# Kernel tuning notes

Measured on AMD Instinct MI355X. Metric: run time of the kernel, lower is better.

The kernel has to match this reference:

```python
import jax, jax.numpy as jnp
import numpy as np

N = 50000          # nodes
E = 400000         # edges
MUL = 32           # multiplicity per irrep
NUM_NEIGHBORS = 8.0
INV_SQRT3 = 1.0 / np.sqrt(3.0)  # w3j(1,1,0) coefficient


def setup_inputs() -> dict:
    key = jax.random.key(0)
    ks = jax.random.split(key, 20)
    inp = {
        # node_input: 32x0e (dim 32) + 32x1o (dim 96) = 128
        "node_input": jax.random.normal(ks[0], (N, 4 * MUL), jnp.float32),
        "node_attr": jnp.ones((N, 1), jnp.float32),           # 1x0e trivial attr
        "edge_src": jax.random.randint(ks[1], (E,), 0, N, jnp.int32),
        "edge_dst": jax.random.randint(ks[2], (E,), 0, N, jnp.int32),
        "edge_attr": jax.random.normal(ks[3], (E, 4), jnp.float32),   # 1x0e + 1x1o
        "edge_scalars": jax.random.normal(ks[4], (E, 16), jnp.float32),
        # FullyConnectedTensorProduct weights (uvw, node_attr has mul 1)
        "w_sc0": jax.random.normal(ks[5], (MUL, MUL), jnp.float32),
        "w_sc1": jax.random.normal(ks[6], (MUL, MUL), jnp.float32),
        "w_lin1_0": jax.random.normal(ks[7], (MUL, MUL), jnp.float32),
        "w_lin1_1": jax.random.normal(ks[8], (MUL, MUL), jnp.float32),
        # radial FC net -> per-edge TP weights (numel = 4*MUL = 128)
        "fc_w1": jax.random.normal(ks[9], (16, 64), jnp.float32),
        "fc_w2": jax.random.normal(ks[10], (64, 4 * MUL), jnp.float32),
        # lin2: irreps_mid (64x0e+64x1o) x attr -> output
        "w_lin2_0": jax.random.normal(ks[11], (2 * MUL, MUL), jnp.float32),
        "w_lin2_1": jax.random.normal(ks[12], (2 * MUL, MUL), jnp.float32),
        # alpha: irreps_mid x attr -> 0e (zero-init in original; small randn for a nontrivial test)
        "w_alpha": 0.1 * jax.random.normal(ks[13], (2 * MUL, 1), jnp.float32),
        # sc_edges: irreps_mid x edge_attr -> edge_attr
        "w_se0a": jax.random.normal(ks[14], (2 * MUL,), jnp.float32),  # mid0e x ea0e -> 0e
        "w_se0b": jax.random.normal(ks[15], (2 * MUL,), jnp.float32),  # mid1o x ea1o -> 0e
        "w_se1a": jax.random.normal(ks[16], (2 * MUL,), jnp.float32),  # mid0e x ea1o -> 1o
        "w_se1b": jax.random.normal(ks[17], (2 * MUL,), jnp.float32),  # mid1o x ea0e -> 1o
    }
    return inp


def reference(node_input, node_attr, edge_src, edge_dst, edge_attr, edge_scalars,
              w_sc0, w_sc1, w_lin1_0, w_lin1_1, fc_w1, fc_w2,
              w_lin2_0, w_lin2_1, w_alpha, w_se0a, w_se0b, w_se1a, w_se1b):
    inv_nn = 1.0 / jnp.sqrt(jnp.asarray(NUM_NEIGHBORS, node_input.dtype))
    n = node_input.shape[0]
    x0 = node_input[:, :MUL]                       # (N, 32)   32x0e
    x1 = node_input[:, MUL:].reshape(n, MUL, 3)    # (N, 32, 3) 32x1o
    a = node_attr                                  # (N, 1)
    s_in = 1.0 / np.sqrt(MUL)                      # FCTP fan-in normalization

    # self-connection: FCTP(input, attr) -> output
    sc0 = (x0 @ w_sc0) * a * s_in
    sc1 = jnp.einsum('num,uw->nwm', x1, w_sc1) * a[:, :, None] * s_in
    node_self = jnp.concatenate([sc0, sc1.reshape(n, 3 * MUL)], axis=1)  # (N, 128)

    # lin1: FCTP(input, attr) -> input irreps
    f0 = (x0 @ w_lin1_0) * a * s_in
    f1 = jnp.einsum('num,uw->nwm', x1, w_lin1_1) * a[:, :, None] * s_in

    # gather source node features per edge
    g0 = f0[edge_src]                              # (E, 32)
    g1 = f1[edge_src]                              # (E, 32, 3)
    ea0 = edge_attr[:, :1]                         # (E, 1)   1x0e
    ea1 = edge_attr[:, 1:]                         # (E, 3)   1x1o

    # radial net -> per-edge TP weights (FullyConnectedNet with sin activation)
    h = jnp.sin(edge_scalars @ fc_w1 * (1.0 / np.sqrt(16.0)))
    w = h @ fc_w2 * (1.0 / np.sqrt(64.0))          # (E, 128)
    wA, wB, wC, wD = jnp.split(w, 4, axis=1)       # each (E, 32)

    # uvu tensor product, 4 instructions
    mA = wA * g0 * ea0                                           # 0e x 0e -> 0e
    mD = wD * jnp.einsum('eum,em->eu', g1, ea1) * INV_SQRT3      # 1o x 1o -> 0e
    mB = (wB * g0)[:, :, None] * ea1[:, None, :]                 # 0e x 1o -> 1o
    mC = (wC[:, :, None] * g1) * ea0[:, :, None]                 # 1o x 0e -> 1o
    mid0 = jnp.concatenate([mA, mD], axis=1)       # (E, 64)  64x0e
    mid1 = jnp.concatenate([mB, mC], axis=1)       # (E, 64, 3) 64x1o

    # scatter-add to destination nodes
    n0 = jax.ops.segment_sum(mid0, edge_dst, num_segments=n) * inv_nn
    n1 = jax.ops.segment_sum(mid1, edge_dst, num_segments=n) * inv_nn

    s_mid = 1.0 / np.sqrt(2 * MUL)
    out0 = (n0 @ w_lin2_0) * a * s_mid
    out1 = jnp.einsum('num,uw->nwm', n1, w_lin2_1) * a[:, :, None] * s_mid
    node_conv = jnp.concatenate([out0, out1.reshape(n, 3 * MUL)], axis=1)

    # alpha gate (sc.output_mask is all ones here, so alpha = 1 - 1 + alpha*1)
    alpha = (n0 @ w_alpha) * a * s_mid             # (N, 1)
    node_conv_out = node_self + alpha * node_conv  # (N, 128)

    # sc_edges: FCTP(mid, edge_attr) -> edge_attr irreps; fan-in = 128 per output
    s_se = 1.0 / np.sqrt(4 * MUL)
    se0 = ((mid0 @ w_se0a) * ea0[:, 0]
           + jnp.einsum('eum,em,u->e', mid1, ea1, w_se0b) * INV_SQRT3) * s_se
    se1 = ((mid0 @ w_se1a)[:, None] * ea1
           + jnp.einsum('eum,u->em', mid1, w_se1b) * ea0) * s_se
    edge_conv_out = edge_attr + jnp.concatenate([se0[:, None], se1], axis=1) * inv_nn

    return node_conv_out, edge_conv_out
```

## Files before the change

kernel.cpp:

```cpp
#include <hip/hip_runtime.h>
#include <math.h>

#define N_NODES 50000
#define E_EDGES 400000

typedef _Float16 f16x2 __attribute__((ext_vector_type(2)));
typedef _Float16 f16x4 __attribute__((ext_vector_type(4)));
typedef _Float16 f16x8 __attribute__((ext_vector_type(8)));

static constexpr float S_IN      = 0.17677669529663687f;
static constexpr float S_MID     = 0.125f;
static constexpr float S_SE      = 0.08838834764831843f;
static constexpr float INV_NN    = 0.35355339059327373f;
static constexpr float INV_SQRT3 = 0.5773502691896258f;
static constexpr float FC1_S     = 0.25f;
static constexpr float FC2_S     = 0.125f;

__device__ inline float dot2(f16x2 a, f16x2 b, float c) {
#if __has_builtin(__builtin_amdgcn_fdot2)
    return __builtin_amdgcn_fdot2(a, b, c, false);
#else
    return c + (float)a[0] * (float)b[0] + (float)a[1] * (float)b[1];
#endif
}

__device__ inline float wave_reduce_dpp(float v) {
    int x;
    x = __builtin_amdgcn_update_dpp(0, __float_as_int(v), 0x111, 0xf, 0xf, true); v += __int_as_float(x);
    x = __builtin_amdgcn_update_dpp(0, __float_as_int(v), 0x112, 0xf, 0xf, true); v += __int_as_float(x);
    x = __builtin_amdgcn_update_dpp(0, __float_as_int(v), 0x114, 0xf, 0xf, true); v += __int_as_float(x);
    x = __builtin_amdgcn_update_dpp(0, __float_as_int(v), 0x118, 0xf, 0xf, true); v += __int_as_float(x);
    x = __builtin_amdgcn_update_dpp(0, __float_as_int(v), 0x142, 0xa, 0xf, true); v += __int_as_float(x);
    x = __builtin_amdgcn_update_dpp(0, __float_as_int(v), 0x143, 0xc, 0xf, true); v += __int_as_float(x);
    return __int_as_float(__builtin_amdgcn_readlane(__float_as_int(v), 63));
}

__global__ __launch_bounds__(256) void node_pre_kernel(
    const float* __restrict__ node_input, const float* __restrict__ node_attr,
    const float* __restrict__ w_sc0, const float* __restrict__ w_sc1,
    const float* __restrict__ w_lin1_0, const float* __restrict__ w_lin1_1,
    float* __restrict__ out_self, float* __restrict__ ws_f)
{
    const int n0 = blockIdx.x * 8;
    const int t  = threadIdx.x;
    __shared__ __align__(16) float sx[8 * 128];
    __shared__ float sa[8];
    ((float4*)sx)[t] = ((const float4*)(node_input + (size_t)n0 * 128))[t];
    if (t < 8) sa[t] = node_attr[n0 + t];
    __syncthreads();

    const int half = t >> 7;
    const int idx  = t & 127;
    float wcol[32];
    int m = 0;
    if (idx < 32) {
        const float* __restrict__ W = half ? w_lin1_0 : w_sc0;
        #pragma unroll
        for (int u = 0; u < 32; ++u) wcol[u] = W[u * 32 + idx];
    } else {
        const float* __restrict__ W = half ? w_lin1_1 : w_sc1;
        const int j = idx - 32;
        const int w = j / 3; m = j % 3;
        #pragma unroll
        for (int u = 0; u < 32; ++u) wcol[u] = W[u * 32 + w];
    }
    float* __restrict__ dstp = half ? ws_f : out_self;
    #pragma unroll
    for (int k = 0; k < 8; ++k) {
        const float* x = sx + k * 128;
        float acc = 0.f;
        if (idx < 32) {
            #pragma unroll
            for (int u = 0; u < 32; ++u) acc += x[u] * wcol[u];
        } else {
            #pragma unroll
            for (int u = 0; u < 32; ++u) acc += x[32 + u * 3 + m] * wcol[u];
        }
        dstp[(size_t)(n0 + k) * 128 + idx] = acc * sa[k] * S_IN;
    }
}

__global__ __launch_bounds__(256) void hist_kernel(
    const int* __restrict__ edge_dst, int* __restrict__ counts)
{
    const int e = blockIdx.x * 256 + threadIdx.x;
    if (e < E_EDGES) atomicAdd(&counts[edge_dst[e]], 1);
}

__global__ __launch_bounds__(1024) void scan_block_kernel(
    const int* __restrict__ counts, int* __restrict__ cursor, int* __restrict__ bsum)
{
    __shared__ int sd[1024];
    const int t   = threadIdx.x;
    const int idx = blockIdx.x * 1024 + t;
    const int c   = (idx < N_NODES) ? counts[idx] : 0;
    sd[t] = c;
    __syncthreads();
    for (int off = 1; off < 1024; off <<= 1) {
        const int v = (t >= off) ? sd[t - off] : 0;
        __syncthreads();
        sd[t] += v;
        __syncthreads();
    }
    if (idx < N_NODES) cursor[idx] = sd[t] - c;
    if (t == 1023) bsum[blockIdx.x] = sd[1023];
}

__global__ void scan_bsum_kernel(const int* __restrict__ bsum, int* __restrict__ boff) {
    if (threadIdx.x == 0) {
        int run = 0;
        for (int b = 0; b < 49; ++b) { boff[b] = run; run += bsum[b]; }
    }
}

__global__ __launch_bounds__(1024) void scan_fixup_kernel(
    int* __restrict__ cursor, const int* __restrict__ boff)
{
    const int idx = blockIdx.x * 1024 + threadIdx.x;
    if (idx < N_NODES) cursor[idx] += boff[blockIdx.x];
}

__global__ __launch_bounds__(256) void scatter_kernel(
    const int* __restrict__ edge_dst, int* __restrict__ cursor,
    int* __restrict__ sorted_eid)
{
    const int e = blockIdx.x * 256 + threadIdx.x;
    if (e < E_EDGES) {
        const int p = atomicAdd(&cursor[edge_dst[e]], 1);
        sorted_eid[p] = e;
    }
}

__global__ __launch_bounds__(256, 4) void edge_kernel(
    const float* __restrict__ ws_f,
    const int* __restrict__ edge_src, const int* __restrict__ edge_dst,
    const float* __restrict__ edge_attr, const float* __restrict__ edge_scalars,
    const float* __restrict__ fc_w1, const float* __restrict__ fc_w2,
    const float* __restrict__ w_se0a, const float* __restrict__ w_se0b,
    const float* __restrict__ w_se1a, const float* __restrict__ w_se1b,
    const int* __restrict__ sorted_eid,
    float* __restrict__ nacc, float* __restrict__ edge_out)
{
    __shared__ __align__(16) _Float16 sW1p[1024];
    __shared__ __align__(16) _Float16 sESh[64 * 22];
    __shared__ __align__(16) _Float16 sW2p[8192];
    __shared__ __align__(16) _Float16 sUN[8192];
    __shared__ __align__(16) float sEA[64 * 4];
    __shared__ int sSRC[64];
    __shared__ int sDST[64];
    __shared__ int sEID[64];

    const int t    = threadIdx.x;
    const int lane = t & 63;
    const int wv   = t >> 6;
    const int e0   = blockIdx.x * 64;

    if (t < 128) {
        const int kp = t >> 4, j4 = (t & 15) * 4;
        float4 a = *(const float4*)&fc_w1[(2 * kp) * 64 + j4];
        float4 b = *(const float4*)&fc_w1[(2 * kp + 1) * 64 + j4];
        f16x8 p;
        p[0]=(_Float16)a.x; p[1]=(_Float16)b.x; p[2]=(_Float16)a.y; p[3]=(_Float16)b.y;
        p[4]=(_Float16)a.z; p[5]=(_Float16)b.z; p[6]=(_Float16)a.w; p[7]=(_Float16)b.w;
        *(f16x8*)&sW1p[(kp * 64 + j4) * 2] = p;
    }
    #pragma unroll
    for (int i = 0; i < 4; ++i) {
        const int u  = t + i * 256;
        const int kp = u >> 5, c4 = (u & 31) * 4;
        float4 a = *(const float4*)&fc_w2[(size_t)(2 * kp) * 128 + c4];
        float4 b = *(const float4*)&fc_w2[(size_t)(2 * kp + 1) * 128 + c4];
        f16x8 p;
        p[0]=(_Float16)a.x; p[1]=(_Float16)b.x; p[2]=(_Float16)a.y; p[3]=(_Float16)b.y;
        p[4]=(_Float16)a.z; p[5]=(_Float16)b.z; p[6]=(_Float16)a.w; p[7]=(_Float16)b.w;
        *(f16x8*)&sW2p[(kp * 128 + c4) * 2] = p;
    }
    {
        const int e = t >> 2, k4 = t & 3;
        const int eid = sorted_eid[e0 + e];
        float4 v = ((const float4*)edge_scalars)[(size_t)eid * 4 + k4];
        f16x2 p0 = {(_Float16)v.x, (_Float16)v.y};
        f16x2 p1 = {(_Float16)v.z, (_Float16)v.w};
        *(f16x2*)&sESh[e * 22 + k4 * 4]     = p0;
        *(f16x2*)&sESh[e * 22 + k4 * 4 + 2] = p1;
    }
    if (t < 64) {
        const int eid = sorted_eid[e0 + t];
        *(float4*)&sEA[t * 4] = ((const float4*)edge_attr)[eid];
        sEID[t] = eid;
    } else if (t < 128) {
        sSRC[t - 64] = edge_src[sorted_eid[e0 + (t - 64)]];
    } else if (t < 192) {
        sDST[t - 128] = edge_dst[sorted_eid[e0 + (t - 128)]];
    }
    __syncthreads();

    _Float16* sHT = sUN;

    {
        const int e = lane, j0 = wv * 16;
        float acc[16];
        #pragma unroll
        for (int i = 0; i < 16; ++i) acc[i] = 0.f;
        #pragma unroll
        for (int kp = 0; kp < 8; ++kp) {
            const f16x2 es2 = *(const f16x2*)&sESh[e * 22 + kp * 2];
            const f16x2* wr = (const f16x2*)&sW1p[(kp * 64 + j0) * 2];
            #pragma unroll
            for (int i = 0; i < 16; ++i) acc[i] = dot2(es2, wr[i], acc[i]);
        }
        #pragma unroll
        for (int i = 0; i < 8; ++i) {
            f16x2 hh = {(_Float16)__sinf(acc[2 * i] * FC1_S),
                        (_Float16)__sinf(acc[2 * i + 1] * FC1_S)};
            *(f16x2*)&sHT[e * 66 + j0 + 2 * i] = hh;
        }
    }
    __syncthreads();

    float wacc[8][4];
    #pragma unroll
    for (int r = 0; r < 8; ++r)
        #pragma unroll
        for (int c = 0; c < 4; ++c) wacc[r][c] = 0.f;
    const int c0 = (t & 31) * 4;
    const int r0 = (t >> 5) * 8;
    for (int kp = 0; kp < 32; ++kp) {
        f16x8 wp8 = *(const f16x8*)&sW2p[(kp * 128 + c0) * 2];
        f16x2 wp[4] = {{wp8[0], wp8[1]}, {wp8[2], wp8[3]},
                       {wp8[4], wp8[5]}, {wp8[6], wp8[7]}};
        f16x2 h2[8];
        #pragma unroll
        for (int r = 0; r < 8; ++r)
            h2[r] = *(const f16x2*)&sHT[(r0 + r) * 66 + kp * 2];
        #pragma unroll
        for (int r = 0; r < 8; ++r)
            #pragma unroll
            for (int c = 0; c < 4; ++c) wacc[r][c] = dot2(h2[r], wp[c], wacc[r][c]);
    }
    __syncthreads();

    _Float16* sWt = sUN;
    {
        #pragma unroll
        for (int r = 0; r < 8; ++r) {
            f16x4 v;
            v[0] = (_Float16)(wacc[r][0] * FC2_S);
            v[1] = (_Float16)(wacc[r][1] * FC2_S);
            v[2] = (_Float16)(wacc[r][2] * FC2_S);
            v[3] = (_Float16)(wacc[r][3] * FC2_S);
            *(f16x4*)&sWt[(r0 + r) * 128 + c0] = v;
        }
    }
    __syncthreads();

    const float se0a = w_se0a[lane], se0b = w_se0b[lane];
    const float se1a = w_se1a[lane], se1b = w_se1b[lane];
    const bool hi = lane >= 32;
    const int  u  = lane - 32;
    const int idxA = hi ? (32 + 3 * u) : lane;
    const int idxB = hi ? (33 + 3 * u) : lane;
    const int idxC = hi ? (34 + 3 * u) : lane;
    const int col1 = hi ? (96 + u) : lane;
    const int col2 = hi ? (64 + u) : (32 + lane);

    int   cur = -1;
    float am0 = 0.f, axx = 0.f, ayy = 0.f, azz = 0.f;

    for (int b = 0; b < 4; ++b) {
        float ga[4], gb[4], gc[4];
        #pragma unroll
        for (int i = 0; i < 4; ++i) {
            const int el = wv * 16 + b * 4 + i;
            const float* fr = ws_f + (size_t)sSRC[el] * 128;
            ga[i] = fr[idxA]; gb[i] = fr[idxB]; gc[i] = fr[idxC];
        }
        #pragma unroll
        for (int i = 0; i < 4; ++i) {
            const int el  = wv * 16 + b * 4 + i;
            const int dst = sDST[el];
            const float ea0 = sEA[el * 4 + 0];
            const float e1x = sEA[el * 4 + 1];
            const float e1y = sEA[el * 4 + 2];
            const float e1z = sEA[el * 4 + 3];
            const float w1v = (float)sWt[el * 128 + col1];
            const float w2v = (float)sWt[el * 128 + col2];

            float mid0, m1x, m1y, m1z;
            if (!hi) {
                mid0 = w1v * ga[i] * ea0;
                const float wbg = w2v * ga[i];
                m1x = wbg * e1x; m1y = wbg * e1y; m1z = wbg * e1z;
            } else {
                const float dot = ga[i] * e1x + gb[i] * e1y + gc[i] * e1z;
                mid0 = w1v * dot * INV_SQRT3;
                const float wce = w2v * ea0;
                m1x = wce * ga[i]; m1y = wce * gb[i]; m1z = wce * gc[i];
            }

            if (dst != cur) {
                if (cur >= 0) {
                    float* np_ = nacc + (size_t)cur * 256;
                    atomicAdd(np_ + lane, am0);
                    atomicAdd(np_ + 64 + lane * 3 + 0, axx);
                    atomicAdd(np_ + 64 + lane * 3 + 1, ayy);
                    atomicAdd(np_ + 64 + lane * 3 + 2, azz);
                }
                cur = dst; am0 = axx = ayy = azz = 0.f;
            }
            am0 += mid0; axx += m1x; ayy += m1y; azz += m1z;

            const float dotm = m1x * e1x + m1y * e1y + m1z * e1z;
            const float s0 = wave_reduce_dpp(mid0 * se0a * ea0 + dotm * se0b * INV_SQRT3);
            const float s1 = wave_reduce_dpp(mid0 * se1a);
            const float s2 = wave_reduce_dpp(m1x * se1b);
            const float s3 = wave_reduce_dpp(m1y * se1b);
            const float s4 = wave_reduce_dpp(m1z * se1b);

            if (lane == 0) {
                float4 o;
                o.x = ea0 + s0 * S_SE * INV_NN;
                o.y = e1x + (s1 * e1x + s2 * ea0) * S_SE * INV_NN;
                o.z = e1y + (s1 * e1y + s3 * ea0) * S_SE * INV_NN;
                o.w = e1z + (s1 * e1z + s4 * ea0) * S_SE * INV_NN;
                *(float4*)&edge_out[(size_t)sEID[el] * 4] = o;
            }
        }
    }
    if (cur >= 0) {
        float* np_ = nacc + (size_t)cur * 256;
        atomicAdd(np_ + lane, am0);
        atomicAdd(np_ + 64 + lane * 3 + 0, axx);
        atomicAdd(np_ + 64 + lane * 3 + 1, ayy);
        atomicAdd(np_ + 64 + lane * 3 + 2, azz);
    }
}

__global__ __launch_bounds__(128) void node_post_kernel(
    const float* __restrict__ nacc, const float* __restrict__ node_attr,
    const float* __restrict__ w_lin2_0, const float* __restrict__ w_lin2_1,
    const float* __restrict__ w_alpha, float* __restrict__ out)
{
    const int n0 = blockIdx.x * 8, t = threadIdx.x;
    __shared__ __align__(16) float sn[8 * 256];
    __shared__ float salpha[8];
    const float4* src = (const float4*)(nacc + (size_t)n0 * 256);
    #pragma unroll
    for (int i = 0; i < 4; ++i) ((float4*)sn)[t + i * 128] = src[t + i * 128];
    __syncthreads();

    if (t < 64) {
        const float wa = w_alpha[t];
        #pragma unroll
        for (int k = 0; k < 8; ++k) {
            const float r = wave_reduce_dpp(sn[k * 256 + t] * wa);
            if (t == 0) salpha[k] = r;
        }
    }
    __syncthreads();

    float wcol[64];
    int m = 0;
    if (t < 32) {
        #pragma unroll
        for (int u = 0; u < 64; ++u) wcol[u] = w_lin2_0[u * 32 + t];
    } else {
        const int j = t - 32; const int w = j / 3; m = j % 3;
        #pragma unroll
        for (int u = 0; u < 64; ++u) wcol[u] = w_lin2_1[u * 32 + w];
    }
    #pragma unroll
    for (int k = 0; k < 8; ++k) {
        const float* s = sn + k * 256;
        float acc = 0.f;
        if (t < 32) {
            #pragma unroll
            for (int u = 0; u < 64; ++u) acc += s[u] * wcol[u];
        } else {
            #pragma unroll
            for (int u = 0; u < 64; ++u) acc += s[64 + u * 3 + m] * wcol[u];
        }
        const float a  = node_attr[n0 + k];
        const float sc = a * S_MID * INV_NN;
        const size_t o = (size_t)(n0 + k) * 128 + t;
        out[o] = out[o] + (salpha[k] * sc) * (acc * sc);
    }
}

extern "C" void kernel_launch(void* const* d_in, const int* in_sizes, int n_in,
                              void* d_out, int out_size, void* d_ws, size_t ws_size,
                              hipStream_t stream)
{
    const float* node_input   = (const float*)d_in[0];
    const float* node_attr    = (const float*)d_in[1];
    const int*   edge_src     = (const int*)d_in[2];
    const int*   edge_dst     = (const int*)d_in[3];
    const float* edge_attr    = (const float*)d_in[4];
    const float* edge_scalars = (const float*)d_in[5];
    const float* w_sc0        = (const float*)d_in[6];
    const float* w_sc1        = (const float*)d_in[7];
    const float* w_lin1_0     = (const float*)d_in[8];
    const float* w_lin1_1     = (const float*)d_in[9];
    const float* fc_w1        = (const float*)d_in[10];
    const float* fc_w2        = (const float*)d_in[11];
    const float* w_lin2_0     = (const float*)d_in[12];
    const float* w_lin2_1     = (const float*)d_in[13];
    const float* w_alpha      = (const float*)d_in[14];
    const float* w_se0a       = (const float*)d_in[15];
    const float* w_se0b       = (const float*)d_in[16];
    const float* w_se1a       = (const float*)d_in[17];
    const float* w_se1b       = (const float*)d_in[18];

    float* out      = (float*)d_out;
    float* edge_out = out + (size_t)N_NODES * 128;

    float* ws_f   = (float*)d_ws;
    float* nacc   = ws_f + (size_t)N_NODES * 128;
    int*   counts = (int*)(nacc + (size_t)N_NODES * 256);
    int*   cursor = counts + N_NODES;
    int*   sid    = cursor + N_NODES;
    int*   bsum   = sid + E_EDGES;
    int*   boff   = bsum + 64;

    hipMemsetAsync(nacc, 0,
        ((size_t)N_NODES * 256 + N_NODES) * sizeof(float), stream);

    node_pre_kernel<<<N_NODES / 8, 256, 0, stream>>>(
        node_input, node_attr, w_sc0, w_sc1, w_lin1_0, w_lin1_1, out, ws_f);

    hist_kernel<<<(E_EDGES + 255) / 256, 256, 0, stream>>>(edge_dst, counts);
    scan_block_kernel<<<49, 1024, 0, stream>>>(counts, cursor, bsum);
    scan_bsum_kernel<<<1, 64, 0, stream>>>(bsum, boff);
    scan_fixup_kernel<<<49, 1024, 0, stream>>>(cursor, boff);
    scatter_kernel<<<(E_EDGES + 255) / 256, 256, 0, stream>>>(edge_dst, cursor, sid);

    edge_kernel<<<E_EDGES / 64, 256, 0, stream>>>(
        ws_f, edge_src, edge_dst, edge_attr, edge_scalars, fc_w1, fc_w2,
        w_se0a, w_se0b, w_se1a, w_se1b, sid, nacc, edge_out);

    node_post_kernel<<<N_NODES / 8, 128, 0, stream>>>(
        nacc, node_attr, w_lin2_0, w_lin2_1, w_alpha, out);
}
```

Baseline: 429.8 us.

## Use MFMA for radial MLP, merge histogram into node_pre, fold bsum scan

The per-edge radial MLP (16->64 sin, 64->128) switches from packed fdot2 loops to 16x16x32 f16 MFMA instructions, with weights transposed and zero-padded in shared memory. The histogram kernel is merged into the node-pre kernel as extra blocks, and the single-thread block-sum scan kernel is replaced by a wave reduction inside the fixup kernel. Together these cut launch count and the ALU cost of the edge MLP. The cost is more shared-memory transpose work during block setup and a padded output stride.

Result: faster. 418.4 us (-2.7%).

```diff
diff --git a/kernel.cpp b/kernel.cpp
--- a/kernel.cpp
+++ b/kernel.cpp
@@ -3,10 +3,13 @@
 
 #define N_NODES 50000
 #define E_EDGES 400000
+#define NPRE_BLOCKS 6250
+#define NHIST_BLOCKS 1563
 
 typedef _Float16 f16x2 __attribute__((ext_vector_type(2)));
 typedef _Float16 f16x4 __attribute__((ext_vector_type(4)));
 typedef _Float16 f16x8 __attribute__((ext_vector_type(8)));
+typedef float    f32x4 __attribute__((ext_vector_type(4)));
 
 static constexpr float S_IN      = 0.17677669529663687f;
 static constexpr float S_MID     = 0.125f;
@@ -15,14 +18,6 @@
 static constexpr float INV_SQRT3 = 0.5773502691896258f;
 static constexpr float FC1_S     = 0.25f;
 static constexpr float FC2_S     = 0.125f;
-
-__device__ inline float dot2(f16x2 a, f16x2 b, float c) {
-#if __has_builtin(__builtin_amdgcn_fdot2)
-    return __builtin_amdgcn_fdot2(a, b, c, false);
-#else
-    return c + (float)a[0] * (float)b[0] + (float)a[1] * (float)b[1];
-#endif
-}
 
 __device__ inline float wave_reduce_dpp(float v) {
     int x;
@@ -35,14 +30,20 @@
     return __int_as_float(__builtin_amdgcn_readlane(__float_as_int(v), 63));
 }
 
-__global__ __launch_bounds__(256) void node_pre_kernel(
+__global__ __launch_bounds__(256) void pre_hist_kernel(
     const float* __restrict__ node_input, const float* __restrict__ node_attr,
     const float* __restrict__ w_sc0, const float* __restrict__ w_sc1,
     const float* __restrict__ w_lin1_0, const float* __restrict__ w_lin1_1,
-    float* __restrict__ out_self, float* __restrict__ ws_f)
-{
+    float* __restrict__ out_self, float* __restrict__ ws_f,
+    const int* __restrict__ edge_dst, int* __restrict__ counts)
+{
+    const int t = threadIdx.x;
+    if (blockIdx.x >= NPRE_BLOCKS) {
+        const int e = (blockIdx.x - NPRE_BLOCKS) * 256 + t;
+        if (e < E_EDGES) atomicAdd(&counts[edge_dst[e]], 1);
+        return;
+    }
     const int n0 = blockIdx.x * 8;
-    const int t  = threadIdx.x;
     __shared__ __align__(16) float sx[8 * 128];
     __shared__ float sa[8];
     ((float4*)sx)[t] = ((const float4*)(node_input + (size_t)n0 * 128))[t];
@@ -80,13 +81,6 @@
     }
 }
 
-__global__ __launch_bounds__(256) void hist_kernel(
-    const int* __restrict__ edge_dst, int* __restrict__ counts)
-{
-    const int e = blockIdx.x * 256 + threadIdx.x;
-    if (e < E_EDGES) atomicAdd(&counts[edge_dst[e]], 1);
-}
-
 __global__ __launch_bounds__(1024) void scan_block_kernel(
     const int* __restrict__ counts, int* __restrict__ cursor, int* __restrict__ bsum)
 {
@@ -106,18 +100,20 @@
     if (t == 1023) bsum[blockIdx.x] = sd[1023];
 }
 
-__global__ void scan_bsum_kernel(const int* __restrict__ bsum, int* __restrict__ boff) {
-    if (threadIdx.x == 0) {
-        int run = 0;
-        for (int b = 0; b < 49; ++b) { boff[b] = run; run += bsum[b]; }
-    }
-}
-
 __global__ __launch_bounds__(1024) void scan_fixup_kernel(
-    int* __restrict__ cursor, const int* __restrict__ boff)
-{
-    const int idx = blockIdx.x * 1024 + threadIdx.x;
-    if (idx < N_NODES) cursor[idx] += boff[blockIdx.x];
+    int* __restrict__ cursor, const int* __restrict__ bsum)
+{
+    __shared__ int boff_s;
+    const int t = threadIdx.x;
+    if (t < 64) {
+        int v = (t < (int)blockIdx.x) ? bsum[t] : 0;
+        #pragma unroll
+        for (int off = 32; off >= 1; off >>= 1) v += __shfl_down(v, off, 64);
+        if (t == 0) boff_s = v;
+    }
+    __syncthreads();
+    const int idx = blockIdx.x * 1024 + t;
+    if (idx < N_NODES) cursor[idx] += boff_s;
 }
 
 __global__ __launch_bounds__(256) void scatter_kernel(
@@ -141,48 +137,52 @@
     const int* __restrict__ sorted_eid,
     float* __restrict__ nacc, float* __restrict__ edge_out)
 {
-    __shared__ __align__(16) _Float16 sW1p[1024];
-    __shared__ __align__(16) _Float16 sESh[64 * 22];
-    __shared__ __align__(16) _Float16 sW2p[8192];
-    __shared__ __align__(16) _Float16 sUN[8192];
+    __shared__ __align__(16) _Float16 sArena[18944];
     __shared__ __align__(16) float sEA[64 * 4];
     __shared__ int sSRC[64];
     __shared__ int sDST[64];
     __shared__ int sEID[64];
 
+    _Float16* __restrict__ sW2T = sArena;
+    _Float16* __restrict__ sHT  = sArena + 9216;
+    _Float16* __restrict__ sES  = sArena + 13824;
+    _Float16* __restrict__ sW1T = sArena + 16384;
+
     const int t    = threadIdx.x;
     const int lane = t & 63;
     const int wv   = t >> 6;
+    const int quad = lane >> 4;
+    const int mm   = lane & 15;
     const int e0   = blockIdx.x * 64;
 
-    if (t < 128) {
-        const int kp = t >> 4, j4 = (t & 15) * 4;
-        float4 a = *(const float4*)&fc_w1[(2 * kp) * 64 + j4];
-        float4 b = *(const float4*)&fc_w1[(2 * kp + 1) * 64 + j4];
-        f16x8 p;
-        p[0]=(_Float16)a.x; p[1]=(_Float16)b.x; p[2]=(_Float16)a.y; p[3]=(_Float16)b.y;
-        p[4]=(_Float16)a.z; p[5]=(_Float16)b.z; p[6]=(_Float16)a.w; p[7]=(_Float16)b.w;
-        *(f16x8*)&sW1p[(kp * 64 + j4) * 2] = p;
+    {
+        const int k = t >> 4, n4 = (t & 15) * 4;
+        float4 v = ((const float4*)fc_w1)[t];
+        sW1T[(n4 + 0) * 40 + k] = (_Float16)v.x;
+        sW1T[(n4 + 1) * 40 + k] = (_Float16)v.y;
+        sW1T[(n4 + 2) * 40 + k] = (_Float16)v.z;
+        sW1T[(n4 + 3) * 40 + k] = (_Float16)v.w;
+        const f16x4 z4 = {(_Float16)0.f, (_Float16)0.f, (_Float16)0.f, (_Float16)0.f};
+        *(f16x4*)&sW1T[(t >> 2) * 40 + 16 + (t & 3) * 4] = z4;
     }
     #pragma unroll
-    for (int i = 0; i < 4; ++i) {
-        const int u  = t + i * 256;
-        const int kp = u >> 5, c4 = (u & 31) * 4;
-        float4 a = *(const float4*)&fc_w2[(size_t)(2 * kp) * 128 + c4];
-        float4 b = *(const float4*)&fc_w2[(size_t)(2 * kp + 1) * 128 + c4];
-        f16x8 p;
-        p[0]=(_Float16)a.x; p[1]=(_Float16)b.x; p[2]=(_Float16)a.y; p[3]=(_Float16)b.y;
-        p[4]=(_Float16)a.z; p[5]=(_Float16)b.z; p[6]=(_Float16)a.w; p[7]=(_Float16)b.w;
-        *(f16x8*)&sW2p[(kp * 128 + c4) * 2] = p;
+    for (int i = 0; i < 8; ++i) {
+        const int u = t + i * 256;
+        const int k = u >> 5, c4 = (u & 31) * 4;
+        float4 v = ((const float4*)fc_w2)[u];
+        sW2T[(c4 + 0) * 72 + k] = (_Float16)v.x;
+        sW2T[(c4 + 1) * 72 + k] = (_Float16)v.y;
+        sW2T[(c4 + 2) * 72 + k] = (_Float16)v.z;
+        sW2T[(c4 + 3) * 72 + k] = (_Float16)v.w;
     }
     {
-        const int e = t >> 2, k4 = t & 3;
+        const int e = t >> 2, k4 = (t & 3) * 4;
         const int eid = sorted_eid[e0 + e];
-        float4 v = ((const float4*)edge_scalars)[(size_t)eid * 4 + k4];
-        f16x2 p0 = {(_Float16)v.x, (_Float16)v.y};
-        f16x2 p1 = {(_Float16)v.z, (_Float16)v.w};
-        *(f16x2*)&sESh[e * 22 + k4 * 4]     = p0;
-        *(f16x2*)&sESh[e * 22 + k4 * 4 + 2] = p1;
+        float4 v = ((const float4*)edge_scalars)[(size_t)eid * 4 + (t & 3)];
+        f16x4 p = {(_Float16)v.x, (_Float16)v.y, (_Float16)v.z, (_Float16)v.w};
+        *(f16x4*)&sES[e * 40 + k4] = p;
+        const f16x4 z4 = {(_Float16)0.f, (_Float16)0.f, (_Float16)0.f, (_Float16)0.f};
+        *(f16x4*)&sES[e * 40 + 16 + k4] = z4;
     }
     if (t < 64) {
         const int eid = sorted_eid[e0 + t];
@@ -195,62 +195,46 @@
     }
     __syncthreads();
 
-    _Float16* sHT = sUN;
-
+    const int eb = wv * 16;
     {
-        const int e = lane, j0 = wv * 16;
-        float acc[16];
-        #pragma unroll
-        for (int i = 0; i < 16; ++i) acc[i] = 0.f;
-        #pragma unroll
-        for (int kp = 0; kp < 8; ++kp) {
-            const f16x2 es2 = *(const f16x2*)&sESh[e * 22 + kp * 2];
-            const f16x2* wr = (const f16x2*)&sW1p[(kp * 64 + j0) * 2];
-            #pragma unroll
-            for (int i = 0; i < 16; ++i) acc[i] = dot2(es2, wr[i], acc[i]);
-        }
-        #pragma unroll
-        for (int i = 0; i < 8; ++i) {
-            f16x2 hh = {(_Float16)__sinf(acc[2 * i] * FC1_S),
-                        (_Float16)__sinf(acc[2 * i + 1] * FC1_S)};
-            *(f16x2*)&sHT[e * 66 + j0 + 2 * i] = hh;
-        }
-    }
-    __syncthreads();
-
-    float wacc[8][4];
-    #pragma unroll
-    for (int r = 0; r < 8; ++r)
-        #pragma unroll
-        for (int c = 0; c < 4; ++c) wacc[r][c] = 0.f;
-    const int c0 = (t & 31) * 4;
-    const int r0 = (t >> 5) * 8;
-    for (int kp = 0; kp < 32; ++kp) {
-        f16x8 wp8 = *(const f16x8*)&sW2p[(kp * 128 + c0) * 2];
-        f16x2 wp[4] = {{wp8[0], wp8[1]}, {wp8[2], wp8[3]},
-                       {wp8[4], wp8[5]}, {wp8[6], wp8[7]}};
-        f16x2 h2[8];
-        #pragma unroll
-        for (int r = 0; r < 8; ++r)
-            h2[r] = *(const f16x2*)&sHT[(r0 + r) * 66 + kp * 2];
-        #pragma unroll
-        for (int r = 0; r < 8; ++r)
-            #pragma unroll
-            for (int c = 0; c < 4; ++c) wacc[r][c] = dot2(h2[r], wp[c], wacc[r][c]);
-    }
-    __syncthreads();
-
-    _Float16* sWt = sUN;
+        const f16x8 a_es = *(const f16x8*)&sES[(eb + mm) * 40 + quad * 8];
+        #pragma unroll
+        for (int jt = 0; jt < 4; ++jt) {
+            const f16x8 b = *(const f16x8*)&sW1T[(jt * 16 + mm) * 40 + quad * 8];
+            f32x4 d = {0.f, 0.f, 0.f, 0.f};
+            d = __builtin_amdgcn_mfma_f32_16x16x32_f16(a_es, b, d, 0, 0, 0);
+            #pragma unroll
+            for (int r = 0; r < 4; ++r)
+                sHT[(eb + quad * 4 + r) * 72 + jt * 16 + mm] =
+                    (_Float16)__sinf(d[r] * FC1_S);
+        }
+    }
+    __syncthreads();
+
+    f32x4 dacc[8];
     {
-        #pragma unroll
-        for (int r = 0; r < 8; ++r) {
-            f16x4 v;
-            v[0] = (_Float16)(wacc[r][0] * FC2_S);
-            v[1] = (_Float16)(wacc[r][1] * FC2_S);
-            v[2] = (_Float16)(wacc[r][2] * FC2_S);
-            v[3] = (_Float16)(wacc[r][3] * FC2_S);
-            *(f16x4*)&sWt[(r0 + r) * 128 + c0] = v;
-        }
+        const f16x8 a_lo = *(const f16x8*)&sHT[(eb + mm) * 72 + quad * 8];
+        const f16x8 a_hi = *(const f16x8*)&sHT[(eb + mm) * 72 + 32 + quad * 8];
+        #pragma unroll
+        for (int ct = 0; ct < 8; ++ct) {
+            const f16x8 b_lo = *(const f16x8*)&sW2T[(ct * 16 + mm) * 72 + quad * 8];
+            const f16x8 b_hi = *(const f16x8*)&sW2T[(ct * 16 + mm) * 72 + 32 + quad * 8];
+            f32x4 d = {0.f, 0.f, 0.f, 0.f};
+            d = __builtin_amdgcn_mfma_f32_16x16x32_f16(a_lo, b_lo, d, 0, 0, 0);
+            d = __builtin_amdgcn_mfma_f32_16x16x32_f16(a_hi, b_hi, d, 0, 0, 0);
+            dacc[ct] = d;
+        }
+    }
+    __syncthreads();
+
+    _Float16* __restrict__ sWt = sArena;
+    {
+        #pragma unroll
+        for (int ct = 0; ct < 8; ++ct)
+            #pragma unroll
+            for (int r = 0; r < 4; ++r)
+                sWt[(eb + quad * 4 + r) * 130 + ct * 16 + mm] =
+                    (_Float16)(dacc[ct][r] * FC2_S);
     }
     __syncthreads();
 
@@ -283,8 +267,8 @@
             const float e1x = sEA[el * 4 + 1];
             const float e1y = sEA[el * 4 + 2];
             const float e1z = sEA[el * 4 + 3];
-            const float w1v = (float)sWt[el * 128 + col1];
-            const float w2v = (float)sWt[el * 128 + col2];
+            const float w1v = (float)sWt[el * 130 + col1];
+            const float w2v = (float)sWt[el * 130 + col2];
 
             float mid0, m1x, m1y, m1z;
             if (!hi) {
@@ -420,18 +404,16 @@
     int*   cursor = counts + N_NODES;
     int*   sid    = cursor + N_NODES;
     int*   bsum   = sid + E_EDGES;
-    int*   boff   = bsum + 64;
 
     hipMemsetAsync(nacc, 0,
         ((size_t)N_NODES * 256 + N_NODES) * sizeof(float), stream);
 
-    node_pre_kernel<<<N_NODES / 8, 256, 0, stream>>>(
-        node_input, node_attr, w_sc0, w_sc1, w_lin1_0, w_lin1_1, out, ws_f);
-
-    hist_kernel<<<(E_EDGES + 255) / 256, 256, 0, stream>>>(edge_dst, counts);
+    pre_hist_kernel<<<NPRE_BLOCKS + NHIST_BLOCKS, 256, 0, stream>>>(
+        node_input, node_attr, w_sc0, w_sc1, w_lin1_0, w_lin1_1, out, ws_f,
+        edge_dst, counts);
+
     scan_block_kernel<<<49, 1024, 0, stream>>>(counts, cursor, bsum);
-    scan_bsum_kernel<<<1, 64, 0, stream>>>(bsum, boff);
-    scan_fixup_kernel<<<49, 1024, 0, stream>>>(cursor, boff);
+    scan_fixup_kernel<<<49, 1024, 0, stream>>>(cursor, bsum);
     scatter_kernel<<<(E_EDGES + 255) / 256, 256, 0, stream>>>(edge_dst, cursor, sid);
 
     edge_kernel<<<E_EDGES / 64, 256, 0, stream>>>(
```
